# Optimization experiments

Measured on AMD Instinct MI355X. Metric: run time of the kernel, lower is better.

The kernel has to match this reference:

```python
import jax, jax.numpy as jnp
import numpy as np

NV, NK, DK, DV, KC = 32, 16, 128, 128, 4  # value heads, key heads, head dims, conv kernel
EPS = 1e-6


def setup_inputs() -> dict:
    key = jax.random.key(0)
    ks = jax.random.split(key, 10)
    B, T, D = 2, 4096, 2048
    key_dim, value_dim = NK * DK, NV * DV
    conv_dim = 2 * key_dim + value_dim
    s = 0.02
    return {
        "hidden_states": jax.random.normal(ks[0], (B, T, D), jnp.float32),
        "W_qkv": jax.random.normal(ks[1], (D, conv_dim), jnp.float32) * s,
        "W_z": jax.random.normal(ks[2], (D, value_dim), jnp.float32) * s,
        "W_b": jax.random.normal(ks[3], (D, NV), jnp.float32) * s,
        "W_a": jax.random.normal(ks[4], (D, NV), jnp.float32) * s,
        "conv_w": jax.random.normal(ks[5], (conv_dim, KC), jnp.float32) * 0.2,
        "dt_bias": jnp.ones((NV,), jnp.float32),
        "A_log": jnp.log(jax.random.uniform(ks[6], (NV,), jnp.float32, 0.5, 16.0)),
        "norm_w": jnp.ones((DV,), jnp.float32),
        "W_out": jax.random.normal(ks[7], (value_dim, D), jnp.float32) * s,
    }


def _silu(x):
    return x * jax.nn.sigmoid(x)


def _l2norm(x):
    return x * jax.lax.rsqrt(jnp.sum(x * x, axis=-1, keepdims=True) + EPS)


def _gated_delta_rule(q, k, v, g, beta):
    # q,k: [B,T,H,DK]; v: [B,T,H,DV]; g,beta: [B,T,H]
    tm = lambda x: jnp.moveaxis(x, 1, 0)  # time-major
    B, T, H = q.shape[0], q.shape[1], q.shape[2]
    S0 = jnp.zeros((B, H, q.shape[-1], v.shape[-1]), q.dtype)

    def step(S, xs):
        qt, kt, vt, gt, bt = xs
        S = S * jnp.exp(gt)[..., None, None]                       # decay
        kS = jnp.einsum('bhk,bhkv->bhv', kt, S)                    # k^T S
        S = S + bt[..., None, None] * kt[..., :, None] * (vt - kS)[..., None, :]
        o = jnp.einsum('bhk,bhkv->bhv', qt, S)
        return S, o

    _, o = jax.lax.scan(step, S0, (tm(q), tm(k), tm(v), tm(g), tm(beta)))
    return jnp.moveaxis(o, 0, 1)  # [B,T,H,DV]


def reference(hidden_states, W_qkv, W_z, W_b, W_a, conv_w, dt_bias, A_log, norm_w, W_out):
    B, T, D = hidden_states.shape
    key_dim, value_dim = NK * DK, NV * DV

    mixed = hidden_states @ W_qkv                                  # [B,T,conv_dim]
    z = (hidden_states @ W_z).reshape(B, T, NV, DV)
    beta = jax.nn.sigmoid(hidden_states @ W_b)                     # [B,T,NV]
    a = hidden_states @ W_a
    g = -jnp.exp(A_log) * jax.nn.softplus(a + dt_bias)             # [B,T,NV]

    # causal depthwise short conv (kernel KC) + silu
    xp = jnp.pad(mixed, ((0, 0), (KC - 1, 0), (0, 0)))
    conv = sum(xp[:, i:i + T, :] * conv_w[:, i] for i in range(KC))
    mixed = _silu(conv)

    q, k, v = jnp.split(mixed, [key_dim, 2 * key_dim], axis=-1)
    q = q.reshape(B, T, NK, DK)
    k = k.reshape(B, T, NK, DK)
    v = v.reshape(B, T, NV, DV)
    rep = NV // NK
    q = jnp.repeat(q, rep, axis=2)
    k = jnp.repeat(k, rep, axis=2)

    q = _l2norm(q) * (DK ** -0.5)
    k = _l2norm(k)

    o = _gated_delta_rule(q, k, v, g, beta)                        # [B,T,NV,DV]

    # fused gated RMSNorm: rmsnorm(o)*w * silu(z)
    var = jnp.mean(o * o, axis=-1, keepdims=True)
    o = o * jax.lax.rsqrt(var + 1e-6) * norm_w * _silu(z)

    return o.reshape(B, T, value_dim) @ W_out
```

## Files before the change

kernel.cpp:

```cpp
#include <hip/hip_runtime.h>
#include <hip/hip_bf16.h>


typedef __attribute__((ext_vector_type(8))) short short8;
typedef __attribute__((ext_vector_type(4))) float f32x4;
typedef unsigned short us;

static __device__ __forceinline__ us f2b(float f) {
  __hip_bfloat16 h = __float2bfloat16(f);
  return __builtin_bit_cast(us, h);
}
static __device__ __forceinline__ float b2f(us u) {
  return __bfloat162float(__builtin_bit_cast(__hip_bfloat16, u));
}
static __device__ __forceinline__ void bar_lds() {
  asm volatile("s_waitcnt lgkmcnt(0)" ::: "memory");
  __builtin_amdgcn_s_barrier();
}

__global__ __launch_bounds__(256) void cvt_f32_bf16(const float* __restrict__ in,
    us* __restrict__ out, long n4) {
  long i = (long)blockIdx.x * 256 + threadIdx.x;
  long stride = (long)gridDim.x * 256;
  for (; i < n4; i += stride) {
    float4 f = reinterpret_cast<const float4*>(in)[i];
    ushort4 u;
    u.x = f2b(f.x); u.y = f2b(f.y); u.z = f2b(f.z); u.w = f2b(f.w);
    reinterpret_cast<ushort4*>(out)[i] = u;
  }
}

__global__ __launch_bounds__(256) void transpose_cvt(const float* __restrict__ in,
    us* __restrict__ out, int K, int N, int Nfull, int coloff, int row_off) {
  __shared__ float tile[64][65];
  int tid = threadIdx.x;
  int n0 = blockIdx.x * 64, k0 = blockIdx.y * 64;
  int tx = tid & 15, ty = tid >> 4;
#pragma unroll
  for (int r = 0; r < 4; ++r) {
    int kk = k0 + ty + r * 16, nn = n0 + tx * 4;
    float4 v = make_float4(0.f, 0.f, 0.f, 0.f);
    if (kk < K && nn < N)
      v = *reinterpret_cast<const float4*>(in + (size_t)kk * Nfull + coloff + nn);
    tile[ty + r * 16][tx * 4 + 0] = v.x;
    tile[ty + r * 16][tx * 4 + 1] = v.y;
    tile[ty + r * 16][tx * 4 + 2] = v.z;
    tile[ty + r * 16][tx * 4 + 3] = v.w;
  }
  __syncthreads();
#pragma unroll
  for (int g = 0; g < 2; ++g) {
    int s = tid + g * 256;
    int nn = s >> 3, ks = (s & 7) * 8;
    if (n0 + nn < N && k0 + ks < K) {
      us ov[8];
#pragma unroll
      for (int i = 0; i < 8; ++i) ov[i] = f2b(tile[ks + i][nn]);
      *reinterpret_cast<uint4*>(out + (size_t)(n0 + nn + row_off) * K + k0 + ks) =
          *reinterpret_cast<uint4*>(ov);
    }
  }
}

template <bool BF16OUT>
__global__ __launch_bounds__(512, 1) void gemm256(const us* __restrict__ A,
    const us* __restrict__ B, void* __restrict__ Cout, int K, int ldC) {
  __shared__ us Abuf[2][256 * 64];
  __shared__ us Bbuf[2][256 * 64];
  int tid = threadIdx.x, w = tid >> 6, lane = tid & 63;
  int wr = w >> 2, wc = w & 3;
  int fr = lane & 15, j4 = lane >> 4;
  int lin = blockIdx.y * gridDim.x + blockIdx.x;
  int nwg = gridDim.x * gridDim.y;
  int wg = (lin & 7) * (nwg >> 3) + (lin >> 3);
  int bx = wg % gridDim.x, by = wg / gridDim.x;
  size_t bm = (size_t)bx * 256, bn = (size_t)by * 256;

  const us *aG[4], *bG[4];
  us *aL[2][4], *bL[2][4];
#pragma unroll
  for (int u = 0; u < 4; ++u) {
    int idx = u * 512 + tid;
    int row = idx >> 3, sl = idx & 7;
    int sg = (sl ^ (row & 7)) * 8;
    aG[u] = A + (bm + row) * K + sg;
    bG[u] = B + (bn + row) * K + sg;
    int lbase = (u * 64 + w * 8) * 64;
#pragma unroll
    for (int bf = 0; bf < 2; ++bf) {
      aL[bf][u] = &Abuf[bf][lbase];
      bL[bf][u] = &Bbuf[bf][lbase];
    }
  }

  f32x4 acc[8][4] = {};
#pragma unroll
  for (int u = 0; u < 4; ++u) {
    __builtin_amdgcn_global_load_lds((const void*)aG[u], (void*)aL[0][u], 16, 0, 0);
    __builtin_amdgcn_global_load_lds((const void*)bG[u], (void*)bL[0][u], 16, 0, 0);
  }
  __syncthreads();

  int nt = K >> 6;
  for (int t = 0; t < nt; ++t) {
    int cur = t & 1, nxt = cur ^ 1;
    const us* Ac = Abuf[cur];
    const us* Bc = Bbuf[cur];
    int kt1 = (t + 1) << 6;
    bool more = (t + 1 < nt);
#pragma unroll
    for (int q = 0; q < 4; ++q) {
      if (more) {
        __builtin_amdgcn_global_load_lds((const void*)(aG[q] + kt1), (void*)aL[nxt][q], 16, 0, 0);
        __builtin_amdgcn_global_load_lds((const void*)(bG[q] + kt1), (void*)bL[nxt][q], 16, 0, 0);
      }
      short8 a0[2], a1[2], bfv[4][2];
      int Ra0 = wr * 128 + 2 * q * 16 + fr;
      int Ra1 = Ra0 + 16;
#pragma unroll
      for (int ks = 0; ks < 2; ++ks) {
        a0[ks] = *reinterpret_cast<const short8*>(&Ac[Ra0 * 64 + (((ks * 4 + j4) ^ (Ra0 & 7)) * 8)]);
        a1[ks] = *reinterpret_cast<const short8*>(&Ac[Ra1 * 64 + (((ks * 4 + j4) ^ (Ra1 & 7)) * 8)]);
#pragma unroll
        for (int fj = 0; fj < 4; ++fj) {
          int Rb = wc * 64 + fj * 16 + fr;
          bfv[fj][ks] = *reinterpret_cast<const short8*>(&Bc[Rb * 64 + (((ks * 4 + j4) ^ (Rb & 7)) * 8)]);
        }
      }
      __builtin_amdgcn_s_setprio(1);
#pragma unroll
      for (int ks = 0; ks < 2; ++ks)
#pragma unroll
        for (int fj = 0; fj < 4; ++fj) {
          acc[2 * q][fj] = __builtin_amdgcn_mfma_f32_16x16x32_bf16(a0[ks], bfv[fj][ks], acc[2 * q][fj], 0, 0, 0);
          acc[2 * q + 1][fj] = __builtin_amdgcn_mfma_f32_16x16x32_bf16(a1[ks], bfv[fj][ks], acc[2 * q + 1][fj], 0, 0, 0);
        }
      __builtin_amdgcn_s_setprio(0);
    }
    __syncthreads();
  }
#pragma unroll
  for (int fi = 0; fi < 8; ++fi)
#pragma unroll
    for (int fj = 0; fj < 4; ++fj) {
      size_t col = bn + wc * 64 + fj * 16 + fr;
#pragma unroll
      for (int e = 0; e < 4; ++e) {
        size_t r = bm + wr * 128 + fi * 16 + j4 * 4 + e;
        size_t off = r * ldC + col;
        if (BF16OUT) reinterpret_cast<us*>(Cout)[off] = f2b(acc[fi][fj][e]);
        else reinterpret_cast<float*>(Cout)[off] = acc[fi][fj][e];
      }
    }
}

__global__ __launch_bounds__(256) void gemm_lds_f32(const us* __restrict__ A,
    const us* __restrict__ B, float* __restrict__ Cout,
    int K, int Nb1, int Nvalid, int ldC) {
  __shared__ us Ash[128 * 64];
  __shared__ us Bsh[128 * 64];
  int tid = threadIdx.x, w = tid >> 6, lane = tid & 63;
  int bm = blockIdx.x * 128, bn = blockIdx.y * 128;
  int wm = (w >> 1) * 64, wn = (w & 1) * 64;
  const us* aP[4]; const us* bP[4]; us* lA[4]; us* lB[4];
#pragma unroll
  for (int i = 0; i < 4; ++i) {
    int idx = i * 256 + tid;
    int row = idx >> 3;
    int sg = ((idx & 7) ^ (row & 7)) * 8;
    aP[i] = A + (size_t)(bm + row) * K + sg;
    int rb = bn + row; if (rb > Nb1) rb = Nb1;
    bP[i] = B + (size_t)rb * K + sg;
    lA[i] = &Ash[(i * 256 + w * 64) * 8];
    lB[i] = &Bsh[(i * 256 + w * 64) * 8];
  }
  f32x4 acc[4][4] = {};
  int fr = lane & 15, j = lane >> 4;
  for (int kt = 0; kt < K; kt += 64) {
#pragma unroll
    for (int i = 0; i < 4; ++i)
      __builtin_amdgcn_global_load_lds((const void*)(aP[i] + kt), (void*)lA[i], 16, 0, 0);
#pragma unroll
    for (int i = 0; i < 4; ++i)
      __builtin_amdgcn_global_load_lds((const void*)(bP[i] + kt), (void*)lB[i], 16, 0, 0);
    __syncthreads();
#pragma unroll
    for (int ks = 0; ks < 2; ++ks) {
      short8 af[4], bfr[4];
#pragma unroll
      for (int f = 0; f < 4; ++f) {
        int Ra = wm + f * 16 + fr;
        af[f] = *reinterpret_cast<const short8*>(&Ash[Ra * 64 + (((ks * 4 + j) ^ (Ra & 7)) * 8)]);
        int Rb = wn + f * 16 + fr;
        bfr[f] = *reinterpret_cast<const short8*>(&Bsh[Rb * 64 + (((ks * 4 + j) ^ (Rb & 7)) * 8)]);
      }
#pragma unroll
      for (int i = 0; i < 4; ++i)
#pragma unroll
        for (int jj = 0; jj < 4; ++jj)
          acc[i][jj] = __builtin_amdgcn_mfma_f32_16x16x32_bf16(af[i], bfr[jj], acc[i][jj], 0, 0, 0);
    }
    __syncthreads();
  }
#pragma unroll
  for (int i = 0; i < 4; ++i)
#pragma unroll
    for (int jj = 0; jj < 4; ++jj) {
      int c0 = bn + wn + jj * 16 + (lane & 15);
      if (c0 < Nvalid) {
#pragma unroll
        for (int e = 0; e < 4; ++e) {
          int r = bm + wm + i * 16 + (lane >> 4) * 4 + e;
          Cout[(size_t)r * ldC + c0] = acc[i][jj][e];
        }
      }
    }
}

template <int MODE>
__global__ __launch_bounds__(256) void conv_chunk(const us* __restrict__ mixed,
    const float* __restrict__ cw, us* __restrict__ outp, int headbase) {
  int bt = blockIdx.x, b = bt >> 12, t = bt & 4095, tid = threadIdx.x;
  int c0 = tid * 8;
  float wv[8][4];
#pragma unroll
  for (int jj = 0; jj < 8; ++jj) {
    float4 w4 = *reinterpret_cast<const float4*>(cw + (size_t)(c0 + jj) * 4);
    wv[jj][0] = w4.x; wv[jj][1] = w4.y; wv[jj][2] = w4.z; wv[jj][3] = w4.w;
  }
  float acc[8] = {};
#pragma unroll
  for (int i = 0; i < 4; ++i) {
    int tt = t - 3 + i;
    if (tt >= 0) {
      us r[8];
      *reinterpret_cast<uint4*>(r) = *reinterpret_cast<const uint4*>(
          mixed + ((size_t)(b * 4096 + tt)) * 2048 + c0);
#pragma unroll
      for (int jj = 0; jj < 8; ++jj) acc[jj] += b2f(r[jj]) * wv[jj][i];
    }
  }
  float x[8];
#pragma unroll
  for (int jj = 0; jj < 8; ++jj) x[jj] = acc[jj] / (1.f + __expf(-acc[jj]));
  us ov[8];
  if (MODE < 2) {
    float s2 = 0.f;
#pragma unroll
    for (int jj = 0; jj < 8; ++jj) s2 += x[jj] * x[jj];
#pragma unroll
    for (int m = 1; m < 16; m <<= 1) s2 += __shfl_xor(s2, m, 64);
    float rn = rsqrtf(s2 + 1e-6f) * (MODE == 0 ? 0.08838834764831845f : 1.f);
#pragma unroll
    for (int jj = 0; jj < 8; ++jj) ov[jj] = f2b(x[jj] * rn);
    int head = tid >> 4, d0 = c0 & 127;
    *reinterpret_cast<uint4*>(outp + ((size_t)bt * 16 + head) * 128 + d0) =
        *reinterpret_cast<uint4*>(ov);
  } else {
#pragma unroll
    for (int jj = 0; jj < 8; ++jj) ov[jj] = f2b(x[jj]);
    *reinterpret_cast<uint4*>(outp + ((size_t)bt * 32 + headbase + (c0 >> 7)) * 128 + (c0 & 127)) =
        *reinterpret_cast<uint4*>(ov);
  }
}

__global__ __launch_bounds__(256) void gates_cumsum(const float* __restrict__ ba,
    const float* __restrict__ dt_bias, const float* __restrict__ A_log,
    float* __restrict__ bl_g, float* __restrict__ beta_g) {
  int widx = blockIdx.x * 4 + (threadIdx.x >> 6);
  int lane = threadIdx.x & 63;
  int bh = widx >> 6, chunk = widx & 63;
  int b = bh >> 5, h = bh & 31;
  size_t btl = (size_t)b * 4096 + chunk * 64 + lane;
  float bv = ba[btl * 64 + h];
  float av = ba[btl * 64 + 32 + h];
  float beta = 1.f / (1.f + __expf(-bv));
  float xx = av + dt_bias[h];
  float sp = (xx > 20.f) ? xx : log1pf(__expf(xx));
  float g = -__expf(A_log[h]) * sp;
#pragma unroll
  for (int off = 1; off < 64; off <<= 1) {
    float n = __shfl_up(g, off, 64);
    if (lane >= off) g += n;
  }
  bl_g[(size_t)widx * 64 + lane] = g;
  beta_g[(size_t)widx * 64 + lane] = beta;
}

static __device__ __forceinline__ f32x4 tile_range(const us* A, int lda,
    const us* B, int ldb, int rt, int ct, int l0, int nk, int lane, f32x4 acc) {
  const us* ar = A + (rt * 16 + (lane & 15)) * lda + l0 * 16 + (lane >> 4) * 8;
  const us* br = B + (ct * 16 + (lane & 15)) * ldb + l0 * 16 + (lane >> 4) * 8;
#pragma unroll
  for (int ks = 0; ks < nk; ++ks) {
    short8 a = *reinterpret_cast<const short8*>(ar + ks * 32);
    short8 bb = *reinterpret_cast<const short8*>(br + ks * 32);
    acc = __builtin_amdgcn_mfma_f32_16x16x32_bf16(a, bb, acc, 0, 0, 0);
  }
  return acc;
}
template <int SA, int SB>
static __device__ __forceinline__ f32x4 tile_swz(const us* A, int lda,
    const us* B, int ldb, int rt, int ct, int nk, int lane, f32x4 acc) {
  int ra = rt * 16 + (lane & 15);
  int rb = ct * 16 + (lane & 15);
  int j = lane >> 4;
#pragma unroll
  for (int ks = 0; ks < nk; ++ks) {
    int slot = j + 4 * ks;
    int oa = (SA >= 0) ? ((slot ^ ((ra >> SA) & 7)) * 8) : (slot * 8);
    int ob = (SB >= 0) ? ((slot ^ ((rb >> SB) & 7)) * 8) : (slot * 8);
    short8 a = *reinterpret_cast<const short8*>(A + ra * lda + oa);
    short8 bb = *reinterpret_cast<const short8*>(B + rb * ldb + ob);
    acc = __builtin_amdgcn_mfma_f32_16x16x32_bf16(a, bb, acc, 0, 0, 0);
  }
  return acc;
}

__global__ __launch_bounds__(512, 1) void scan_p1(
    const us* __restrict__ k, const float* __restrict__ bl_g,
    const float* __restrict__ beta_g, us* __restrict__ Tg) {
  __shared__ us Kb[64 * 136];
  __shared__ us Ebt[64 * 72];
  __shared__ us W1[64 * 72], W1t[64 * 72], W3[64 * 72];
  __shared__ float bl_s[64], bet_s[64];
  us* const Eb = Kb;

  int bid = blockIdx.x, bh = bid >> 6, c = bid & 63;
  int b = bh >> 5, h = bh & 31, hk = h >> 1;
  int tid = threadIdx.x, w = tid >> 6, lane = tid & 63;
  int row = tid >> 3, c16 = (tid & 7) * 16;
  size_t bt0 = (size_t)b * 4096 + c * 64;

  const int TR_[10] = {0, 1, 1, 2, 2, 2, 3, 3, 3, 3};
  const int TC_[10] = {0, 0, 1, 0, 1, 2, 0, 1, 2, 3};

  const us* kp = k + ((bt0 + row) * 16 + hk) * 128 + c16;
  uint4 kr0 = reinterpret_cast<const uint4*>(kp)[0];
  uint4 kr1 = reinterpret_cast<const uint4*>(kp)[1];
  int gbase = (bh * 64 + c) * 64;
  if (tid < 64) { bl_s[tid] = bl_g[gbase + tid]; bet_s[tid] = beta_g[gbase + tid]; }
  *reinterpret_cast<uint4*>(&Kb[row * 136 + c16]) = kr0;
  *reinterpret_cast<uint4*>(&Kb[row * 136 + c16 + 8]) = kr1;
  __syncthreads();
  {
    int art = w & 3;
#pragma unroll
    for (int s = 0; s < 2; ++s) {
      int ct = (w >> 2) * 2 + s;
      f32x4 a = tile_range(Kb, 136, Kb, 136, art, ct, 0, 4, lane, f32x4{});
#pragma unroll
      for (int e = 0; e < 4; ++e) {
        int tr = art * 16 + (lane >> 4) * 4 + e;
        int cl = ct * 16 + (lane & 15);
        float dv = (cl < tr) ? bet_s[tr] * __expf(bl_s[tr] - bl_s[cl]) * a[e] : 0.f;
        W1[tr * 72 + cl] = f2b(dv);
        W1t[cl * 72 + tr] = f2b(dv);
        W3[tr * 72 + cl] = f2b((tr == cl ? 1.f : 0.f) - dv);
      }
    }
  }
  __syncthreads();
  f32x4 freg[2] = {};
#pragma unroll
  for (int it = 1; it <= 5; ++it) {
    if (it > 1) {
#pragma unroll
      for (int s = 0; s < 2; ++s) {
        int j = w + s * 8;
        if (j < 10) {
          int r = TR_[j], cc0 = TC_[j];
#pragma unroll
          for (int e = 0; e < 4; ++e) {
            int rr = r * 16 + (lane >> 4) * 4 + e, cl = cc0 * 16 + (lane & 15);
            W3[rr * 72 + cl] = f2b(b2f(W3[rr * 72 + cl]) + freg[s][e]);
          }
        }
      }
    }
    if (it == 1) {
      const int ZR[12] = {0, 0, 0, 1, 1, 2, 1, 2, 2, 3, 3, 3};
      const int ZC[12] = {1, 2, 3, 2, 3, 3, 0, 0, 1, 0, 1, 2};
#pragma unroll
      for (int u = 0; u < 12; ++u) {
        if ((u & 7) != w) continue;
        us* arr = (u < 6) ? Eb : Ebt;
        if (lane < 32) {
          int rr = ZR[u] * 16 + (lane >> 1);
          *reinterpret_cast<uint4*>(&arr[rr * 72 + ZC[u] * 16 + (lane & 1) * 8]) =
              make_uint4(0, 0, 0, 0);
        }
      }
    }
    const us* Es  = (it & 1) ? W1  : Eb;
    const us* Est = (it & 1) ? W1t : Ebt;
    us* Ed  = (it & 1) ? Eb  : W1;
    us* Edt = (it & 1) ? Ebt : W1t;
#pragma unroll
    for (int s = 0; s < 2; ++s) {
      int j = w + s * 8;
      if (j < 10) {
        int r = TR_[j], cc0 = TC_[j];
        int l0 = cc0 & ~1, nk = (r - l0 + 2) >> 1;
        f32x4 a = tile_range(Es, 72, Est, 72, r, cc0, l0, nk, lane, f32x4{});
#pragma unroll
        for (int e = 0; e < 4; ++e) {
          int rr = r * 16 + (lane >> 4) * 4 + e, cl = cc0 * 16 + (lane & 15);
          us val = f2b(a[e]);
          Ed[rr * 72 + cl] = val;
          Edt[cl * 72 + rr] = val;
        }
      }
    }
    __syncthreads();
    const us* Ent = (it & 1) ? Ebt : W1t;
#pragma unroll
    for (int s = 0; s < 2; ++s) {
      int j = w + s * 8;
      if (j < 10) {
        int r = TR_[j], cc0 = TC_[j];
        int l0 = cc0 & ~1, nk = (r - l0 + 2) >> 1;
        freg[s] = tile_range(W3, 72, Ent, 72, r, cc0, l0, nk, lane, f32x4{});
      }
    }
    __syncthreads();
  }
#pragma unroll
  for (int s = 0; s < 2; ++s) {
    int j = w + s * 8;
    if (j < 10) {
      int r = TR_[j], cc0 = TC_[j];
#pragma unroll
      for (int e = 0; e < 4; ++e) {
        int rr = r * 16 + (lane >> 4) * 4 + e, cl = cc0 * 16 + (lane & 15);
        W3[rr * 72 + cl] = f2b(b2f(W3[rr * 72 + cl]) + freg[s][e]);
      }
    }
  }
  __syncthreads();
  *reinterpret_cast<uint4*>(&Tg[(size_t)bid * 4096 + tid * 8]) =
      *reinterpret_cast<const uint4*>(&W3[row * 72 + (tid & 7) * 8]);
}

__global__ __launch_bounds__(512, 1) void scan_p2(
    const us* __restrict__ q, const us* __restrict__ k, const us* __restrict__ v,
    const float* __restrict__ bl_g, const float* __restrict__ beta_g,
    const us* __restrict__ Tg, us* __restrict__ o) {
  __shared__ us Sb[32 * 136];
  __shared__ us Kb[64 * 136];
  __shared__ us Qb[64 * 136];
  __shared__ us Ktb[128 * 72];
  __shared__ us Vt[32 * 72];
  __shared__ us Ut[32 * 72];
  __shared__ us W3[64 * 72];
  __shared__ us WP[64 * 72];
  __shared__ float bl_s[64], bet_s[64], ksc_s[64];

  int bid = blockIdx.x, vs = bid >> 6, bh = bid & 63;
  int b = bh >> 5, h = bh & 31, hk = h >> 1;
  int tid = threadIdx.x, w = tid >> 6, lane = tid & 63;
  int row = tid >> 3, c16 = (tid & 7) * 16;

  for (int i = tid; i < (32 * 136) / 8; i += 512)
    reinterpret_cast<uint4*>(Sb)[i] = make_uint4(0, 0, 0, 0);
  __syncthreads();

  uint4 kr0, kr1, qr0, qr1, vr, Tr;
  float blr, blC, bet, betv;
  int vrow = (tid & 255) >> 2, vseg = tid & 3;
  auto load_regs = [&](int c) {
    size_t bt0 = (size_t)b * 4096 + c * 64;
    const us* kp = k + ((bt0 + row) * 16 + hk) * 128 + c16;
    const us* qp = q + ((bt0 + row) * 16 + hk) * 128 + c16;
    kr0 = reinterpret_cast<const uint4*>(kp)[0];
    kr1 = reinterpret_cast<const uint4*>(kp)[1];
    qr0 = reinterpret_cast<const uint4*>(qp)[0];
    qr1 = reinterpret_cast<const uint4*>(qp)[1];
    Tr = *reinterpret_cast<const uint4*>(&Tg[((size_t)bh * 64 + c) * 4096 + tid * 8]);
    int gbase = (bh * 64 + c) * 64;
    blr = bl_g[gbase + row];
    blC = bl_g[gbase + 63];
    bet = beta_g[gbase + row];
    if (tid < 256) {
      vr = *reinterpret_cast<const uint4*>(
          v + ((bt0 + vrow) * 32 + h) * 128 + vs * 32 + vseg * 8);
      betv = beta_g[gbase + vrow];
    }
  };
  load_regs(0);

  for (int c = 0; c < 64; ++c) {
    size_t bt0 = (size_t)b * 4096 + c * 64;
    if ((tid & 7) == 0) {
      bl_s[row] = blr; bet_s[row] = bet;
      ksc_s[row] = __expf(blC - blr);
    }
    *reinterpret_cast<uint4*>(&Kb[row * 136 + c16]) = kr0;
    *reinterpret_cast<uint4*>(&Kb[row * 136 + c16 + 8]) = kr1;
    *reinterpret_cast<uint4*>(&Qb[row * 136 + c16]) = qr0;
    *reinterpret_cast<uint4*>(&Qb[row * 136 + c16 + 8]) = qr1;
    *reinterpret_cast<uint4*>(&W3[row * 72 + (tid & 7) * 8]) = Tr;
    if (tid < 256) {
      us vreg[8];
      *reinterpret_cast<uint4*>(vreg) = vr;
#pragma unroll
      for (int i = 0; i < 8; ++i) {
        int vv = vseg * 8 + i;
        Vt[vv * 72 + (((vrow >> 3) ^ vseg) & 7) * 8 + (vrow & 7)] = f2b(betv * b2f(vreg[i]));
      }
    }
    load_regs(c < 63 ? c + 1 : 63);
    bar_lds();
#pragma unroll
    for (int tk = 0; tk < 2; ++tk) {
      int task = tid + tk * 512;
      int d = task & 127, oct = task >> 7;
      us kt[8];
#pragma unroll
      for (int i = 0; i < 8; ++i)
        kt[i] = f2b(ksc_s[oct * 8 + i] * b2f(Kb[(oct * 8 + i) * 136 + d]));
      *reinterpret_cast<uint4*>(&Ktb[d * 72 + ((oct ^ ((d >> 4) & 7)) * 8)]) =
          *reinterpret_cast<uint4*>(kt);
    }
    int rtO = w >> 1, ctv = w & 1;
    f32x4 o1 = tile_swz<-1, -1>(Qb, 136, Sb, 136, rtO, ctv, 4, lane, f32x4{});
    {
      int art = w & 3;
#pragma unroll
      for (int s = 0; s < 2; ++s) {
        int ct = (w >> 2) * 2 + s;
        f32x4 a = tile_swz<-1, -1>(Qb, 136, Kb, 136, art, ct, 4, lane, f32x4{});
#pragma unroll
        for (int e = 0; e < 4; ++e) {
          int tr = art * 16 + (lane >> 4) * 4 + e;
          int cl = ct * 16 + (lane & 15);
          float pv = (cl <= tr) ? __expf(bl_s[tr] - bl_s[cl]) * a[e] : 0.f;
          WP[tr * 72 + cl] = f2b(pv);
        }
      }
    }
    {
      int vrt = w >> 2, ct = w & 3;
      f32x4 a = tile_swz<-1, -1>(Sb, 136, Kb, 136, vrt, ct, 4, lane, f32x4{});
      int tt = ct * 16 + (lane & 15);
      float csc = bet_s[tt] * __expf(bl_s[tt]);
#pragma unroll
      for (int e = 0; e < 4; ++e) {
        int vv = vrt * 16 + (lane >> 4) * 4 + e;
        int off = vv * 72 + (((tt >> 3) ^ ((vv >> 3) & 7)) * 8) + (tt & 7);
        Vt[off] = f2b(b2f(Vt[off]) - csc * a[e]);
      }
    }
    bar_lds();
    {
      int vrt = w >> 2, ct = w & 3;
      f32x4 a = tile_swz<3, -1>(Vt, 72, W3, 72, vrt, ct, 2, lane, f32x4{});
#pragma unroll
      for (int e = 0; e < 4; ++e) {
        int uv = vrt * 16 + (lane >> 4) * 4 + e;
        int ut2 = ct * 16 + (lane & 15);
        Ut[uv * 72 + (((ut2 >> 3) ^ ((uv >> 3) & 7)) * 8) + (ut2 & 7)] = f2b(a[e]);
      }
    }
    bar_lds();
    float lamC = __expf(bl_s[63]);
    {
      f32x4 a = tile_swz<-1, 3>(WP, 72, Ut, 72, rtO, ctv, 2, lane, f32x4{});
#pragma unroll
      for (int e = 0; e < 4; ++e) {
        int tt = rtO * 16 + (lane >> 4) * 4 + e;
        int vv = vs * 32 + ctv * 16 + (lane & 15);
        float val = __expf(bl_s[tt]) * o1[e] + a[e];
        o[((bt0 + tt) * 32 + h) * 128 + vv] = f2b(val);
      }
    }
#pragma unroll
    for (int s = 0; s < 2; ++s) {
      int ti = w * 2 + s;
      int vrt = ti >> 3, dt = ti & 7;
      f32x4 a = tile_swz<3, 4>(Ut, 72, Ktb, 72, vrt, dt, 2, lane, f32x4{});
#pragma unroll
      for (int e = 0; e < 4; ++e) {
        int vv = vrt * 16 + (lane >> 4) * 4 + e, dd = dt * 16 + (lane & 15);
        Sb[vv * 136 + dd] = f2b(lamC * b2f(Sb[vv * 136 + dd]) + a[e]);
      }
    }
    bar_lds();
  }
}

__global__ __launch_bounds__(256) void rms_gate(us* oy,
    const us* __restrict__ z, const float* __restrict__ nw) {
  int sub = threadIdx.x & 31;
  size_t row = (size_t)blockIdx.x * 8 + (threadIdx.x >> 5);
  size_t base = row * 128 + sub * 4;
  ushort4 ov = *reinterpret_cast<ushort4*>(oy + base);
  ushort4 zv = *reinterpret_cast<const ushort4*>(z + base);
  float o_[4] = {b2f(ov.x), b2f(ov.y), b2f(ov.z), b2f(ov.w)};
  float ss = o_[0] * o_[0] + o_[1] * o_[1] + o_[2] * o_[2] + o_[3] * o_[3];
#pragma unroll
  for (int m = 1; m < 32; m <<= 1) ss += __shfl_xor(ss, m, 64);
  float r = rsqrtf(ss * (1.f / 128.f) + 1e-6f);
  float4 w4 = *reinterpret_cast<const float4*>(nw + sub * 4);
  float zz[4] = {b2f(zv.x), b2f(zv.y), b2f(zv.z), b2f(zv.w)};
  float wv[4] = {w4.x, w4.y, w4.z, w4.w};
  us res[4];
#pragma unroll
  for (int i = 0; i < 4; ++i) {
    float zs = zz[i] / (1.f + __expf(-zz[i]));
    res[i] = f2b(o_[i] * r * wv[i] * zs);
  }
  *reinterpret_cast<ushort4*>(oy + base) = *reinterpret_cast<ushort4*>(res);
}

extern "C" void kernel_launch(void* const* d_in, const int* in_sizes, int n_in,
                              void* d_out, int out_size, void* d_ws, size_t ws_size,
                              hipStream_t stream) {
  const float* hs      = (const float*)d_in[0];
  const float* W_qkv   = (const float*)d_in[1];
  const float* W_z     = (const float*)d_in[2];
  const float* W_b     = (const float*)d_in[3];
  const float* W_a     = (const float*)d_in[4];
  const float* conv_w  = (const float*)d_in[5];
  const float* dt_bias = (const float*)d_in[6];
  const float* A_log   = (const float*)d_in[7];
  const float* norm_w  = (const float*)d_in[8];
  const float* W_out   = (const float*)d_in[9];
  float* out = (float*)d_out;

  char* ws = (char*)d_ws;
  const size_t MiB = 1u << 20;
  float* ba_buf = (float*)(ws);
  float* bl_g   = (float*)(ws + 2 * MiB);
  float* bt_g   = (float*)(ws + 3 * MiB);
  us*    wt     = (us*)(ws + 4 * MiB);
  us*    Tg     = (us*)(ws + 4 * MiB);
  us*    mixed  = (us*)(ws + 36 * MiB);
  us*    o_buf  = (us*)(ws + 36 * MiB);
  us*    hs_bf0 = (us*)(ws + 68 * MiB);
  us*    q_buf  = (us*)(ws + 100 * MiB);
  us*    hs_bf1 = q_buf;
  us*    k_buf  = (us*)(ws + 132 * MiB);
  us*    v_buf  = (us*)(ws + 164 * MiB);
  us*    z_bf   = v_buf;

  cvt_f32_bf16<<<2048, 256, 0, stream>>>(hs, hs_bf0, (long)8192 * 2048 / 4);

  for (int c = 0; c < 4; ++c) {
    transpose_cvt<<<dim3(32, 32), 256, 0, stream>>>(W_qkv, wt, 2048, 2048, 8192, c * 2048, 0);
    gemm256<true><<<dim3(32, 8), 512, 0, stream>>>(hs_bf0, wt, mixed, 2048, 2048);
    const float* cwc = conv_w + (size_t)c * 2048 * 4;
    if (c == 0)      conv_chunk<0><<<8192, 256, 0, stream>>>(mixed, cwc, q_buf, 0);
    else if (c == 1) conv_chunk<1><<<8192, 256, 0, stream>>>(mixed, cwc, k_buf, 0);
    else if (c == 2) conv_chunk<2><<<8192, 256, 0, stream>>>(mixed, cwc, v_buf, 0);
    else             conv_chunk<2><<<8192, 256, 0, stream>>>(mixed, cwc, v_buf, 16);
  }
  transpose_cvt<<<dim3(1, 32), 256, 0, stream>>>(W_b, wt, 2048, 32, 32, 0, 0);
  transpose_cvt<<<dim3(1, 32), 256, 0, stream>>>(W_a, wt, 2048, 32, 32, 0, 32);
  gemm_lds_f32<<<dim3(64, 1), 256, 0, stream>>>(hs_bf0, wt, ba_buf, 2048, 63, 64, 64);
  gates_cumsum<<<1024, 256, 0, stream>>>(ba_buf, dt_bias, A_log, bl_g, bt_g);
  scan_p1<<<4096, 512, 0, stream>>>(k_buf, bl_g, bt_g, Tg);
  scan_p2<<<256, 512, 0, stream>>>(q_buf, k_buf, v_buf, bl_g, bt_g, Tg, o_buf);
  cvt_f32_bf16<<<2048, 256, 0, stream>>>(hs, hs_bf1, (long)8192 * 2048 / 4);
  transpose_cvt<<<dim3(64, 32), 256, 0, stream>>>(W_z, wt, 2048, 4096, 4096, 0, 0);
  gemm256<true><<<dim3(32, 16), 512, 0, stream>>>(hs_bf1, wt, z_bf, 2048, 4096);
  rms_gate<<<32768, 256, 0, stream>>>(o_buf, z_bf, norm_w);
  transpose_cvt<<<dim3(32, 64), 256, 0, stream>>>(W_out, wt, 4096, 2048, 2048, 0, 0);
  gemm256<false><<<dim3(32, 8), 512, 0, stream>>>(o_buf, wt, out, 4096, 2048);
}
```

Before: 1.235 ms.

## Split GEMM tile loads into staged halves with partial vmcnt waits

Reorders the global-to-LDS loads of the main bf16 GEMM so the A rows needed by the first half of the k-step (sub-tiles 0 and 2) and all of B are issued first. The full __syncthreads at the start and end of each k-step is replaced by s_waitcnt vmcnt waits plus raw barriers. The first half of the MFMA work can then begin once only part of the tile has landed, with a second barrier mid-iteration before the remaining A rows are used. This aims to shorten the stall on load latency, but relies on exact vmcnt counting and the LDS write-after-read ordering being correct.

```diff
diff --git a/kernel.cpp b/kernel.cpp
--- a/kernel.cpp
+++ b/kernel.cpp
@@ -94,12 +94,14 @@
   }
 
   f32x4 acc[8][4] = {};
-#pragma unroll
-  for (int u = 0; u < 4; ++u) {
-    __builtin_amdgcn_global_load_lds((const void*)aG[u], (void*)aL[0][u], 16, 0, 0);
-    __builtin_amdgcn_global_load_lds((const void*)bG[u], (void*)bL[0][u], 16, 0, 0);
-  }
-  __syncthreads();
+  __builtin_amdgcn_global_load_lds((const void*)aG[0], (void*)aL[0][0], 16, 0, 0);
+  __builtin_amdgcn_global_load_lds((const void*)aG[2], (void*)aL[0][2], 16, 0, 0);
+  __builtin_amdgcn_global_load_lds((const void*)bG[0], (void*)bL[0][0], 16, 0, 0);
+  __builtin_amdgcn_global_load_lds((const void*)bG[1], (void*)bL[0][1], 16, 0, 0);
+  __builtin_amdgcn_global_load_lds((const void*)bG[2], (void*)bL[0][2], 16, 0, 0);
+  __builtin_amdgcn_global_load_lds((const void*)bG[3], (void*)bL[0][3], 16, 0, 0);
+  __builtin_amdgcn_global_load_lds((const void*)aG[1], (void*)aL[0][1], 16, 0, 0);
+  __builtin_amdgcn_global_load_lds((const void*)aG[3], (void*)aL[0][3], 16, 0, 0);
 
   int nt = K >> 6;
   for (int t = 0; t < nt; ++t) {
@@ -108,19 +110,37 @@
     const us* Bc = Bbuf[cur];
     int kt1 = (t + 1) << 6;
     bool more = (t + 1 < nt);
+    asm volatile("s_waitcnt vmcnt(2)" ::: "memory");
+    __builtin_amdgcn_s_barrier();
 #pragma unroll
     for (int q = 0; q < 4; ++q) {
+      if (q == 2) {
+        if (more) { asm volatile("s_waitcnt vmcnt(4)" ::: "memory"); }
+        else      { asm volatile("s_waitcnt vmcnt(0)" ::: "memory"); }
+        __builtin_amdgcn_s_barrier();
+      }
       if (more) {
-        __builtin_amdgcn_global_load_lds((const void*)(aG[q] + kt1), (void*)aL[nxt][q], 16, 0, 0);
-        __builtin_amdgcn_global_load_lds((const void*)(bG[q] + kt1), (void*)bL[nxt][q], 16, 0, 0);
-      }
-      short8 a0[2], a1[2], bfv[4][2];
+        if (q == 0) {
+          __builtin_amdgcn_global_load_lds((const void*)(aG[0] + kt1), (void*)aL[nxt][0], 16, 0, 0);
+          __builtin_amdgcn_global_load_lds((const void*)(aG[2] + kt1), (void*)aL[nxt][2], 16, 0, 0);
+        } else if (q == 1) {
+          __builtin_amdgcn_global_load_lds((const void*)(bG[0] + kt1), (void*)bL[nxt][0], 16, 0, 0);
+          __builtin_amdgcn_global_load_lds((const void*)(bG[1] + kt1), (void*)bL[nxt][1], 16, 0, 0);
+        } else if (q == 2) {
+          __builtin_amdgcn_global_load_lds((const void*)(bG[2] + kt1), (void*)bL[nxt][2], 16, 0, 0);
+          __builtin_amdgcn_global_load_lds((const void*)(bG[3] + kt1), (void*)bL[nxt][3], 16, 0, 0);
+        } else {
+          __builtin_amdgcn_global_load_lds((const void*)(aG[1] + kt1), (void*)aL[nxt][1], 16, 0, 0);
+          __builtin_amdgcn_global_load_lds((const void*)(aG[3] + kt1), (void*)aL[nxt][3], 16, 0, 0);
+        }
+      }
+      short8 a0v[2], a1v[2], bfv[4][2];
       int Ra0 = wr * 128 + 2 * q * 16 + fr;
       int Ra1 = Ra0 + 16;
 #pragma unroll
       for (int ks = 0; ks < 2; ++ks) {
-        a0[ks] = *reinterpret_cast<const short8*>(&Ac[Ra0 * 64 + (((ks * 4 + j4) ^ (Ra0 & 7)) * 8)]);
-        a1[ks] = *reinterpret_cast<const short8*>(&Ac[Ra1 * 64 + (((ks * 4 + j4) ^ (Ra1 & 7)) * 8)]);
+        a0v[ks] = *reinterpret_cast<const short8*>(&Ac[Ra0 * 64 + (((ks * 4 + j4) ^ (Ra0 & 7)) * 8)]);
+        a1v[ks] = *reinterpret_cast<const short8*>(&Ac[Ra1 * 64 + (((ks * 4 + j4) ^ (Ra1 & 7)) * 8)]);
 #pragma unroll
         for (int fj = 0; fj < 4; ++fj) {
           int Rb = wc * 64 + fj * 16 + fr;
@@ -132,12 +152,11 @@
       for (int ks = 0; ks < 2; ++ks)
 #pragma unroll
         for (int fj = 0; fj < 4; ++fj) {
-          acc[2 * q][fj] = __builtin_amdgcn_mfma_f32_16x16x32_bf16(a0[ks], bfv[fj][ks], acc[2 * q][fj], 0, 0, 0);
-          acc[2 * q + 1][fj] = __builtin_amdgcn_mfma_f32_16x16x32_bf16(a1[ks], bfv[fj][ks], acc[2 * q + 1][fj], 0, 0, 0);
+          acc[2 * q][fj] = __builtin_amdgcn_mfma_f32_16x16x32_bf16(a0v[ks], bfv[fj][ks], acc[2 * q][fj], 0, 0, 0);
+          acc[2 * q + 1][fj] = __builtin_amdgcn_mfma_f32_16x16x32_bf16(a1v[ks], bfv[fj][ks], acc[2 * q + 1][fj], 0, 0, 0);
         }
       __builtin_amdgcn_s_setprio(0);
     }
-    __syncthreads();
   }
 #pragma unroll
   for (int fi = 0; fi < 8; ++fi)
```

New measurement: 1.284 ms. +4.0%, slower.
